# Kernel tuning notes

Hardware: AMD Instinct MI355X
Metric: run time of the kernel (lower is better)

Reference implementation:

```python
import jax, jax.numpy as jnp
import numpy as np

N_BLOCKS = 16
BLOCK = 512  # filters per conv layer
N = N_BLOCKS * BLOCK  # 8192 total nodes (filters)
E = 128  # embedding_feature_len
LAYER_NUM = 2
NEG = -9e15  # matches -9000000000000000.0 zero_vec


def _build_adj():
    filter_num = [BLOCK] * N_BLOCKS
    adj = np.zeros((N, N), dtype=np.float32)
    row = last = filter_num[0]
    for num in filter_num:
        adj[row:row + num, row - last:row] = 1.0
        row += num
        last = num
    np.fill_diagonal(adj, 0.0)
    return adj


def setup_inputs() -> dict:
    key = jax.random.key(0)
    k_h, k_w0, k_w1 = jax.random.split(key, 3)
    h = jax.random.normal(k_h, (N, E), dtype=jnp.float32)
    adj = jnp.asarray(_build_adj())
    s = 1.0 / np.sqrt(E)
    W0 = jax.random.normal(k_w0, (E, E), dtype=jnp.float32) * s
    b0 = jnp.zeros((E,), dtype=jnp.float32)
    W1 = jax.random.normal(k_w1, (E, E), dtype=jnp.float32) * s
    b1 = jnp.zeros((E,), dtype=jnp.float32)
    return {"h": h, "adj": adj, "W0": W0, "b0": b0, "W1": W1, "b1": b1}


def _gat_layer(h, adj, W, b):
    n, e = h.shape
    # attention = h @ h.T / sqrt(E)
    att = jnp.matmul(h, h.T) / jnp.sqrt(jnp.asarray(e, h.dtype))
    A = jnp.where(adj > 0, att, jnp.asarray(NEG, h.dtype))
    A = jax.nn.softmax(A, axis=1)
    # A = (A + I) / 2, without materializing a dense NxN eye
    d = jnp.arange(n)
    A = A * 0.5
    A = A.at[d, d].add(0.5)
    # rows [:num_filter_1layer] overridden with identity rows
    nf1 = jnp.sum(adj[:, 0] != 0)
    mask = d < nf1  # [N]
    A = jnp.where(mask[:, None], 0.0, A)
    A = A.at[d, d].set(jnp.where(mask, 1.0, A[d, d]))
    h_new = jnp.matmul(h, W.T) + b  # nn.Linear
    return jax.nn.relu(jnp.matmul(A, h_new))


def reference(h, adj, W0, b0, W1, b1):
    x = _gat_layer(h, adj, W0, b0)
    x = _gat_layer(x, adj, W1, b1)
    return x
```

## Files before the change

kernel.cpp:

```cpp
#include <hip/hip_runtime.h>

typedef __attribute__((ext_vector_type(4))) float f32x4;
typedef __attribute__((ext_vector_type(8))) short s16x8;
typedef unsigned int u32;
typedef __attribute__((ext_vector_type(2))) u32 u32x2;
typedef __attribute__((ext_vector_type(4))) u32 u32x4;

#define NN 8192
#define EE 128
#define SCLOG2E 0.12751743f

__device__ __forceinline__ ushort f2bf(float f){
  u32 u = __builtin_bit_cast(u32, f);
  u += 0x7fffu + ((u >> 16) & 1u);
  return (ushort)(u >> 16);
}
__device__ __forceinline__ float bf2f(ushort h){
  u32 u = ((u32)h) << 16;
  return __builtin_bit_cast(float, u);
}
__device__ __forceinline__ void gload16(const void* g, void* l){
  __builtin_amdgcn_global_load_lds((const __attribute__((address_space(1))) u32*)g,
                                   (__attribute__((address_space(3))) u32*)l, 16, 0, 0);
}
#define VM_WAIT0   do{ asm volatile("s_waitcnt vmcnt(0)" ::: "memory"); __builtin_amdgcn_sched_barrier(0);}while(0)
#define LGKM_WAIT0 do{ asm volatile("s_waitcnt lgkmcnt(0)" ::: "memory"); __builtin_amdgcn_sched_barrier(0);}while(0)

__global__ __launch_bounds__(256) void prep_k(const float* __restrict__ h,
                                              const float* __restrict__ W0,
                                              const float* __restrict__ W1,
                                              ushort* __restrict__ hhi,
                                              ushort* __restrict__ w0h, ushort* __restrict__ w1h){
  const int b = blockIdx.x, t = threadIdx.x;
  if (b < 128){
    const int base = b*64*EE;
    #pragma unroll
    for (int i=0;i<16;++i){
      int idx = (i*256 + t)*2;
      float2 v = *(const float2*)&h[base + idx];
      *(u32*)&hhi[base + idx] = (u32)f2bf(v.x) | ((u32)f2bf(v.y) << 16);
    }
  } else {
    const float* Ws = (b==128) ? W0 : W1;
    ushort* Wd = (b==128) ? w0h : w1h;
    #pragma unroll
    for (int i=0;i<32;++i){
      int idx = (i*256 + t)*2;
      float2 v = *(const float2*)&Ws[idx];
      *(u32*)&Wd[idx] = (u32)f2bf(v.x) | ((u32)f2bf(v.y) << 16);
    }
  }
}

template<int LAYER>
__global__ __launch_bounds__(256, 1) void gat_k(
    const ushort* __restrict__ Qsrc,
    const ushort* __restrict__ Xsrc,
    const ushort* __restrict__ Wb, const float* __restrict__ bias,
    ushort* __restrict__ Ybf,
    float* __restrict__ Yf)
{
  __shared__ __align__(16) char smem[76288];
  const int t = threadIdx.x;
  const int wv = t >> 6, l = t & 63, lr = l & 15, lg = l >> 4;
  const int wid = ((blockIdx.x & 7) << 5) | (blockIdx.x >> 3);
  const u32 chkoff = wv*8192;
  char* PB = smem + 65536 + wv*2560;
  float* Ls = (float*)(smem + 75776);
  char* AG = smem + 65536;

  const int idx = wid - 16;
  const int rb = (wid < 16) ? wid*32 : 512 + (idx>>4)*512 + (idx&15)*32;
  s16x8 af[2][4];

  if (wid >= 16){
    const int pbase = (idx >> 4) * 512;

    s16x8 qh[2][4];
    #pragma unroll
    for (int h2=0;h2<2;++h2)
      #pragma unroll
      for (int kb=0;kb<4;++kb)
        qh[h2][kb] = *(const s16x8*)&Qsrc[(rb+h2*16+lr)*EE + kb*32 + lg*8];

    const ushort* srcrow = &Xsrc[((l>>3)*4 + ((l&7)>>1))*EE + (l&1)*8];
    auto stage = [&](int c){
      const ushort* src = srcrow + (pbase + c*32)*EE;
      #pragma unroll
      for (int it=0; it<8; ++it)
        gload16(src + it*16, smem + chkoff + it*1024);
    };

    f32x4 O[2][8];
    #pragma unroll
    for (int h2=0;h2<2;++h2)
      #pragma unroll
      for (int nt=0;nt<8;++nt) O[h2][nt] = (f32x4){0.f,0.f,0.f,0.f};
    float lsum[2][4] = {{0.f,0.f,0.f,0.f},{0.f,0.f,0.f,0.f}};

    const u32 trbase = chkoff + (u32)((l>>4)*256 + (l&15)*8);

    stage(wv*4);
    for (int tc=0; tc<4; ++tc){
      VM_WAIT0;

      s16x8 kf[2][4];
      #pragma unroll
      for (int pt=0;pt<2;++pt)
        #pragma unroll
        for (int kb=0;kb<4;++kb)
          kf[pt][kb] = *(const s16x8*)(smem + chkoff + (kb*2+(lg>>1))*1024
                         + (pt*4 + (lr>>2))*128 + (lr&3)*32 + (lg&1)*16);

      s16x8 vf[8];
      #pragma unroll
      for (int nt=0;nt<8;++nt){
        u32x2 a, b;
        u32 off = trbase + (u32)(nt*1024);
        asm volatile("ds_read_b64_tr_b16 %0, %2\n\t"
                     "ds_read_b64_tr_b16 %1, %2 offset:128"
                     : "=&v"(a), "=&v"(b) : "v"(off));
        u32x4 c4; c4[0]=a[0]; c4[1]=a[1]; c4[2]=b[0]; c4[3]=b[1];
        vf[nt] = __builtin_bit_cast(s16x8, c4);
      }
      LGKM_WAIT0;
      if (tc < 3) stage(wv*4 + tc + 1);

      f32x4 sv[2][2];
      __builtin_amdgcn_s_setprio(1);
      #pragma unroll
      for (int h2=0;h2<2;++h2)
        #pragma unroll
        for (int pt=0;pt<2;++pt){
          f32x4 s = (f32x4){0.f,0.f,0.f,0.f};
          #pragma unroll
          for (int kb=0;kb<4;++kb)
            s = __builtin_amdgcn_mfma_f32_16x16x32_bf16(qh[h2][kb], kf[pt][kb], s, 0,0,0);
          sv[h2][pt] = s;
        }
      __builtin_amdgcn_s_setprio(0);

      #pragma unroll
      for (int h2=0;h2<2;++h2)
        #pragma unroll
        for (int r=0;r<4;++r){
          float e0 = exp2f(sv[h2][0][r]*SCLOG2E);
          float e1 = exp2f(sv[h2][1][r]*SCLOG2E);
          sv[h2][0][r] = e0; sv[h2][1][r] = e1;
          lsum[h2][r] += e0 + e1;
        }
      #pragma unroll
      for (int h2=0;h2<2;++h2)
        #pragma unroll
        for (int pt=0;pt<2;++pt)
          #pragma unroll
          for (int r=0;r<4;++r)
            *(ushort*)(PB + h2*1280 + (lg*4+r)*80 + (lr + pt*16)*2) = f2bf(sv[h2][pt][r]);
      s16x8 pf[2];
      #pragma unroll
      for (int h2=0;h2<2;++h2)
        pf[h2] = *(const s16x8*)(PB + h2*1280 + lr*80 + lg*16);
      __builtin_amdgcn_s_setprio(1);
      #pragma unroll
      for (int h2=0;h2<2;++h2)
        #pragma unroll
        for (int nt=0;nt<8;++nt)
          O[h2][nt] = __builtin_amdgcn_mfma_f32_16x16x32_bf16(pf[h2], vf[nt], O[h2][nt], 0,0,0);
      __builtin_amdgcn_s_setprio(0);
    }

    #pragma unroll
    for (int h2=0;h2<2;++h2)
      #pragma unroll
      for (int r=0;r<4;++r){
        float s = lsum[h2][r];
        #pragma unroll
        for (int off=1; off<16; off<<=1) s += __shfl_xor(s, off, 16);
        lsum[h2][r] = s;
      }
    #pragma unroll
    for (int h2=0;h2<2;++h2)
      #pragma unroll
      for (int nt=0;nt<8;++nt)
        *(f32x4*)(smem + h2*32768 + wv*8192 + nt*1024 + l*16) = O[h2][nt];
    if (lr == 0){
      #pragma unroll
      for (int h2=0;h2<2;++h2)
        #pragma unroll
        for (int r=0;r<4;++r) Ls[h2*64 + wv*16 + lg*4 + r] = lsum[h2][r];
    }
    __syncthreads();

    f32x4 om[2][2][4];
    #pragma unroll
    for (int h2=0;h2<2;++h2)
      #pragma unroll
      for (int ntl=0;ntl<2;++ntl){
        int nt = wv*2 + ntl;
        #pragma unroll
        for (int r2=0;r2<4;++r2)
          om[h2][ntl][r2] = *(const f32x4*)(smem + h2*32768 + r2*8192 + nt*1024 + l*16);
      }
    float L[2][4];
    #pragma unroll
    for (int h2=0;h2<2;++h2)
      #pragma unroll
      for (int r=0;r<4;++r){
        int q = lg*4 + r;
        L[h2][r] = Ls[h2*64+q] + Ls[h2*64+16+q] + Ls[h2*64+32+q] + Ls[h2*64+48+q];
      }
    __syncthreads();

    #pragma unroll
    for (int h2=0;h2<2;++h2)
      #pragma unroll
      for (int ntl=0;ntl<2;++ntl){
        int nt = wv*2 + ntl;
        int col = nt*16 + lr;
        #pragma unroll
        for (int r=0;r<4;++r){
          int row = rb + h2*16 + lg*4 + r;
          float qc = bf2f(Qsrc[row*EE + col]);
          float s4 = om[h2][ntl][0][r]+om[h2][ntl][1][r]+om[h2][ntl][2][r]+om[h2][ntl][3][r];
          float agg = 0.5f*qc + 0.5f*(s4 / L[h2][r]);
          int q = h2*16 + lg*4 + r;
          *(ushort*)(AG + q*256 + (((col>>3) ^ (q&7))*16) + (col&7)*2) = f2bf(agg);
        }
      }
    __syncthreads();
    #pragma unroll
    for (int h2=0;h2<2;++h2)
      #pragma unroll
      for (int kb=0;kb<4;++kb)
        af[h2][kb] = *(const s16x8*)(AG + (h2*16+lr)*256 + (((kb*4+lg) ^ (lr&7))*16));
  } else {
    #pragma unroll
    for (int h2=0;h2<2;++h2)
      #pragma unroll
      for (int kb=0;kb<4;++kb)
        af[h2][kb] = *(const s16x8*)&Qsrc[(rb + h2*16 + lr)*EE + kb*32 + lg*8];
  }

  f32x4 acc[2][2];
  #pragma unroll
  for (int h2=0;h2<2;++h2){ acc[h2][0]=(f32x4){0.f,0.f,0.f,0.f}; acc[h2][1]=(f32x4){0.f,0.f,0.f,0.f}; }
  #pragma unroll
  for (int ntl=0;ntl<2;++ntl)
    #pragma unroll
    for (int kb=0;kb<4;++kb){
      s16x8 wb = *(const s16x8*)&Wb[(wv*32 + ntl*16 + lr)*EE + kb*32 + lg*8];
      #pragma unroll
      for (int h2=0;h2<2;++h2)
        acc[h2][ntl] = __builtin_amdgcn_mfma_f32_16x16x32_bf16(af[h2][kb], wb, acc[h2][ntl], 0,0,0);
    }
  #pragma unroll
  for (int h2=0;h2<2;++h2)
    #pragma unroll
    for (int ntl=0;ntl<2;++ntl){
      int col = wv*32 + ntl*16 + lr;
      float bv = bias[col];
      #pragma unroll
      for (int r=0;r<4;++r){
        int row = rb + h2*16 + lg*4 + r;
        float v = fmaxf(acc[h2][ntl][r] + bv, 0.f);
        if constexpr (LAYER == 1) Ybf[row*EE + col] = f2bf(v);
        else                      Yf[row*EE + col] = v;
      }
    }
}

extern "C" void kernel_launch(void* const* d_in, const int* in_sizes, int n_in,
                              void* d_out, int out_size, void* d_ws, size_t ws_size,
                              hipStream_t stream) {
  const float* h  = (const float*)d_in[0];
  const float* W0 = (const float*)d_in[2];
  const float* b0 = (const float*)d_in[3];
  const float* W1 = (const float*)d_in[4];
  const float* b1 = (const float*)d_in[5];
  float* out = (float*)d_out;

  ushort* hhi  = (ushort*)d_ws;
  ushort* w0h  = hhi  + NN*EE;
  ushort* w1h  = w0h  + EE*EE;
  ushort* X1hi = w1h  + EE*EE;

  prep_k<<<130, 256, 0, stream>>>(h, W0, W1, hhi, w0h, w1h);
  gat_k<1><<<256, 256, 0, stream>>>(hhi, hhi, w0h, b0, X1hi, nullptr);
  gat_k<2><<<256, 256, 0, stream>>>(X1hi, X1hi, w1h, b1, nullptr, out);
}
```

Before: 30.42 us.

## Fuse layer-2 identity rows into layer-1 kernel and shrink layer-2 grid

The first 512 rows are identity rows in both layers, so layer 1 now finishes them: it writes its bf16 output into a swizzled LDS tile, runs the second linear (W1, b1) with ReLU, and stores the final fp32 output directly. Layer 2 then launches only 240 blocks, all on the banded attention rows, and its block-to-row mapping is changed to match. The prep kernel is split into twice as many smaller blocks to spread the bf16 conversion over more CUs. This cuts layer-2 launch size and tail work, at the cost of extra work and a barrier in 16 of the layer-1 blocks.

```diff
diff --git a/kernel.cpp b/kernel.cpp
--- a/kernel.cpp
+++ b/kernel.cpp
@@ -32,17 +32,17 @@
                                               ushort* __restrict__ hhi,
                                               ushort* __restrict__ w0h, ushort* __restrict__ w1h){
   const int b = blockIdx.x, t = threadIdx.x;
-  if (b < 128){
-    const int base = b*64*EE;
-    #pragma unroll
-    for (int i=0;i<16;++i){
+  if (b < 256){
+    const int base = b*32*EE;
+    #pragma unroll
+    for (int i=0;i<8;++i){
       int idx = (i*256 + t)*2;
       float2 v = *(const float2*)&h[base + idx];
       *(u32*)&hhi[base + idx] = (u32)f2bf(v.x) | ((u32)f2bf(v.y) << 16);
     }
   } else {
-    const float* Ws = (b==128) ? W0 : W1;
-    ushort* Wd = (b==128) ? w0h : w1h;
+    const float* Ws = (b==256) ? W0 : W1;
+    ushort* Wd = (b==256) ? w0h : w1h;
     #pragma unroll
     for (int i=0;i<32;++i){
       int idx = (i*256 + t)*2;
@@ -57,23 +57,27 @@
     const ushort* __restrict__ Qsrc,
     const ushort* __restrict__ Xsrc,
     const ushort* __restrict__ Wb, const float* __restrict__ bias,
+    const ushort* __restrict__ W2b, const float* __restrict__ bias2,
     ushort* __restrict__ Ybf,
     float* __restrict__ Yf)
 {
   __shared__ __align__(16) char smem[76288];
   const int t = threadIdx.x;
   const int wv = t >> 6, l = t & 63, lr = l & 15, lg = l >> 4;
-  const int wid = ((blockIdx.x & 7) << 5) | (blockIdx.x >> 3);
+  const int bid = blockIdx.x;
+  const int wid = (LAYER == 1) ? (((bid & 7) << 5) | (bid >> 3))
+                               : ((bid & 7)*30 + (bid >> 3));
   const u32 chkoff = wv*8192;
   char* PB = smem + 65536 + wv*2560;
   float* Ls = (float*)(smem + 75776);
   char* AG = smem + 65536;
 
-  const int idx = wid - 16;
-  const int rb = (wid < 16) ? wid*32 : 512 + (idx>>4)*512 + (idx&15)*32;
+  const int idx = (LAYER == 1) ? wid - 16 : wid;
+  const bool banded = (LAYER == 2) || (wid >= 16);
+  const int rb = banded ? 512 + (idx>>4)*512 + (idx&15)*32 : wid*32;
   s16x8 af[2][4];
 
-  if (wid >= 16){
+  if (banded){
     const int pbase = (idx >> 4) * 512;
 
     s16x8 qh[2][4];
@@ -263,10 +267,54 @@
       for (int r=0;r<4;++r){
         int row = rb + h2*16 + lg*4 + r;
         float v = fmaxf(acc[h2][ntl][r] + bv, 0.f);
-        if constexpr (LAYER == 1) Ybf[row*EE + col] = f2bf(v);
-        else                      Yf[row*EE + col] = v;
-      }
-    }
+        if constexpr (LAYER == 1){
+          ushort hi = f2bf(v);
+          Ybf[row*EE + col] = hi;
+          if (!banded){
+            int q = h2*16 + lg*4 + r;
+            *(ushort*)(AG + q*256 + (((col>>3) ^ (q&7))*16) + (col&7)*2) = hi;
+          }
+        } else {
+          Yf[row*EE + col] = v;
+        }
+      }
+    }
+
+  if constexpr (LAYER == 1){
+    if (!banded){
+      __syncthreads();
+      s16x8 af2[2][4];
+      #pragma unroll
+      for (int h2=0;h2<2;++h2)
+        #pragma unroll
+        for (int kb=0;kb<4;++kb)
+          af2[h2][kb] = *(const s16x8*)(AG + (h2*16+lr)*256 + (((kb*4+lg) ^ (lr&7))*16));
+      f32x4 a2[2][2];
+      #pragma unroll
+      for (int h2=0;h2<2;++h2){ a2[h2][0]=(f32x4){0.f,0.f,0.f,0.f}; a2[h2][1]=(f32x4){0.f,0.f,0.f,0.f}; }
+      #pragma unroll
+      for (int ntl=0;ntl<2;++ntl)
+        #pragma unroll
+        for (int kb=0;kb<4;++kb){
+          s16x8 wb = *(const s16x8*)&W2b[(wv*32 + ntl*16 + lr)*EE + kb*32 + lg*8];
+          #pragma unroll
+          for (int h2=0;h2<2;++h2)
+            a2[h2][ntl] = __builtin_amdgcn_mfma_f32_16x16x32_bf16(af2[h2][kb], wb, a2[h2][ntl], 0,0,0);
+        }
+      #pragma unroll
+      for (int h2=0;h2<2;++h2)
+        #pragma unroll
+        for (int ntl=0;ntl<2;++ntl){
+          int col = wv*32 + ntl*16 + lr;
+          float bv = bias2[col];
+          #pragma unroll
+          for (int r=0;r<4;++r){
+            int row = rb + h2*16 + lg*4 + r;
+            Yf[row*EE + col] = fmaxf(a2[h2][ntl][r] + bv, 0.f);
+          }
+        }
+    }
+  }
 }
 
 extern "C" void kernel_launch(void* const* d_in, const int* in_sizes, int n_in,
@@ -284,7 +332,7 @@
   ushort* w1h  = w0h  + EE*EE;
   ushort* X1hi = w1h  + EE*EE;
 
-  prep_k<<<130, 256, 0, stream>>>(h, W0, W1, hhi, w0h, w1h);
-  gat_k<1><<<256, 256, 0, stream>>>(hhi, hhi, w0h, b0, X1hi, nullptr);
-  gat_k<2><<<256, 256, 0, stream>>>(X1hi, X1hi, w1h, b1, nullptr, out);
-}
+  prep_k<<<258, 256, 0, stream>>>(h, W0, W1, hhi, w0h, w1h);
+  gat_k<1><<<256, 256, 0, stream>>>(hhi, hhi, w0h, b0, w1h, b1, X1hi, out);
+  gat_k<2><<<240, 256, 0, stream>>>(X1hi, X1hi, w1h, b1, nullptr, nullptr, nullptr, out);
+}
```

New measurement: 31.36 us. 3.1% more time.

## Fuse fp32-to-bf16 conversion into GAT kernels and drop prep kernel

Applied to the files above, without the earlier changes.

Removes the separate prep kernel that converted h and the weights to bf16. Layer 1 now loads fp32 h directly, converting in registers and writing bf16 into LDS with a register double-buffered staging pipeline instead of async global-to-LDS loads. Both layers convert the fp32 weights on the fly. This saves one kernel launch and a full round trip of h through memory, at the cost of more VGPR pressure, redundant conversion of the same rows across blocks, and a loss of the async LDS loads in layer 1.

```diff
diff --git a/kernel.cpp b/kernel.cpp
--- a/kernel.cpp
+++ b/kernel.cpp
@@ -25,40 +25,15 @@
 }
 #define VM_WAIT0   do{ asm volatile("s_waitcnt vmcnt(0)" ::: "memory"); __builtin_amdgcn_sched_barrier(0);}while(0)
 #define LGKM_WAIT0 do{ asm volatile("s_waitcnt lgkmcnt(0)" ::: "memory"); __builtin_amdgcn_sched_barrier(0);}while(0)
-
-__global__ __launch_bounds__(256) void prep_k(const float* __restrict__ h,
-                                              const float* __restrict__ W0,
-                                              const float* __restrict__ W1,
-                                              ushort* __restrict__ hhi,
-                                              ushort* __restrict__ w0h, ushort* __restrict__ w1h){
-  const int b = blockIdx.x, t = threadIdx.x;
-  if (b < 128){
-    const int base = b*64*EE;
-    #pragma unroll
-    for (int i=0;i<16;++i){
-      int idx = (i*256 + t)*2;
-      float2 v = *(const float2*)&h[base + idx];
-      *(u32*)&hhi[base + idx] = (u32)f2bf(v.x) | ((u32)f2bf(v.y) << 16);
-    }
-  } else {
-    const float* Ws = (b==128) ? W0 : W1;
-    ushort* Wd = (b==128) ? w0h : w1h;
-    #pragma unroll
-    for (int i=0;i<32;++i){
-      int idx = (i*256 + t)*2;
-      float2 v = *(const float2*)&Ws[idx];
-      *(u32*)&Wd[idx] = (u32)f2bf(v.x) | ((u32)f2bf(v.y) << 16);
-    }
-  }
-}
+#define CODE_FENCE do{ asm volatile("" ::: "memory"); __builtin_amdgcn_sched_barrier(0);}while(0)
 
 template<int LAYER>
 __global__ __launch_bounds__(256, 1) void gat_k(
-    const ushort* __restrict__ Qsrc,
-    const ushort* __restrict__ Xsrc,
-    const ushort* __restrict__ Wb, const float* __restrict__ bias,
+    const float*  __restrict__ hf,
+    const ushort* __restrict__ Xbf,
+    const float*  __restrict__ Wf, const float* __restrict__ bias,
     ushort* __restrict__ Ybf,
-    float* __restrict__ Yf)
+    float*  __restrict__ Yf)
 {
   __shared__ __align__(16) char smem[76288];
   const int t = threadIdx.x;
@@ -80,17 +55,53 @@
     #pragma unroll
     for (int h2=0;h2<2;++h2)
       #pragma unroll
-      for (int kb=0;kb<4;++kb)
-        qh[h2][kb] = *(const s16x8*)&Qsrc[(rb+h2*16+lr)*EE + kb*32 + lg*8];
-
-    const ushort* srcrow = &Xsrc[((l>>3)*4 + ((l&7)>>1))*EE + (l&1)*8];
-    auto stage = [&](int c){
-      const ushort* src = srcrow + (pbase + c*32)*EE;
+      for (int kb=0;kb<4;++kb){
+        if constexpr (LAYER == 1){
+          f32x4 a0 = *(const f32x4*)&hf[(rb+h2*16+lr)*EE + kb*32 + lg*8];
+          f32x4 a1 = *(const f32x4*)&hf[(rb+h2*16+lr)*EE + kb*32 + lg*8 + 4];
+          #pragma unroll
+          for (int j=0;j<4;++j){
+            qh[h2][kb][j]   = (short)f2bf(a0[j]);
+            qh[h2][kb][j+4] = (short)f2bf(a1[j]);
+          }
+        } else {
+          qh[h2][kb] = *(const s16x8*)&Xbf[(rb+h2*16+lr)*EE + kb*32 + lg*8];
+        }
+      }
+
+    const int srow = (l>>3)*4 + ((l&7)>>1);
+    const int scol = (l&1)*8;
+
+    const ushort* srcrow2 = (LAYER == 2) ? &Xbf[srow*EE + scol] : nullptr;
+    auto stage2 = [&](int c){
+      const ushort* src = srcrow2 + (pbase + c*32)*EE;
       #pragma unroll
       for (int it=0; it<8; ++it)
         gload16(src + it*16, smem + chkoff + it*1024);
     };
 
+    const float* srcrow1 = (LAYER == 1) ? &hf[srow*EE + scol] : nullptr;
+    f32x4 stg[8][2];
+    auto ldissue = [&](int c){
+      const float* src = srcrow1 + (pbase + c*32)*EE;
+      #pragma unroll
+      for (int it=0; it<8; ++it){
+        stg[it][0] = *(const f32x4*)(src + it*16);
+        stg[it][1] = *(const f32x4*)(src + it*16 + 4);
+      }
+    };
+    auto cvwrite = [&](){
+      #pragma unroll
+      for (int it=0; it<8; ++it){
+        u32x4 pk;
+        pk[0] = (u32)f2bf(stg[it][0][0]) | ((u32)f2bf(stg[it][0][1]) << 16);
+        pk[1] = (u32)f2bf(stg[it][0][2]) | ((u32)f2bf(stg[it][0][3]) << 16);
+        pk[2] = (u32)f2bf(stg[it][1][0]) | ((u32)f2bf(stg[it][1][1]) << 16);
+        pk[3] = (u32)f2bf(stg[it][1][2]) | ((u32)f2bf(stg[it][1][3]) << 16);
+        *(u32x4*)(smem + chkoff + it*1024 + l*16) = pk;
+      }
+    };
+
     f32x4 O[2][8];
     #pragma unroll
     for (int h2=0;h2<2;++h2)
@@ -100,9 +111,17 @@
 
     const u32 trbase = chkoff + (u32)((l>>4)*256 + (l&15)*8);
 
-    stage(wv*4);
+    if constexpr (LAYER == 1){
+      ldissue(wv*4);
+      cvwrite();
+      ldissue(wv*4 + 1);
+      CODE_FENCE;
+    } else {
+      stage2(wv*4);
+    }
+
     for (int tc=0; tc<4; ++tc){
-      VM_WAIT0;
+      if constexpr (LAYER == 2) VM_WAIT0;
 
       s16x8 kf[2][4];
       #pragma unroll
@@ -124,7 +143,16 @@
         vf[nt] = __builtin_bit_cast(s16x8, c4);
       }
       LGKM_WAIT0;
-      if (tc < 3) stage(wv*4 + tc + 1);
+
+      if constexpr (LAYER == 1){
+        if (tc < 3){
+          cvwrite();
+          if (tc < 2) ldissue(wv*4 + tc + 2);
+          CODE_FENCE;
+        }
+      } else {
+        if (tc < 3) stage2(wv*4 + tc + 1);
+      }
 
       f32x4 sv[2][2];
       __builtin_amdgcn_s_setprio(1);
@@ -220,7 +248,9 @@
         #pragma unroll
         for (int r=0;r<4;++r){
           int row = rb + h2*16 + lg*4 + r;
-          float qc = bf2f(Qsrc[row*EE + col]);
+          float qc;
+          if constexpr (LAYER == 1) qc = hf[row*EE + col];
+          else                      qc = bf2f(Xbf[row*EE + col]);
           float s4 = om[h2][ntl][0][r]+om[h2][ntl][1][r]+om[h2][ntl][2][r]+om[h2][ntl][3][r];
           float agg = 0.5f*qc + 0.5f*(s4 / L[h2][r]);
           int q = h2*16 + lg*4 + r;
@@ -237,8 +267,19 @@
     #pragma unroll
     for (int h2=0;h2<2;++h2)
       #pragma unroll
-      for (int kb=0;kb<4;++kb)
-        af[h2][kb] = *(const s16x8*)&Qsrc[(rb + h2*16 + lr)*EE + kb*32 + lg*8];
+      for (int kb=0;kb<4;++kb){
+        if constexpr (LAYER == 1){
+          f32x4 a0 = *(const f32x4*)&hf[(rb+h2*16+lr)*EE + kb*32 + lg*8];
+          f32x4 a1 = *(const f32x4*)&hf[(rb+h2*16+lr)*EE + kb*32 + lg*8 + 4];
+          #pragma unroll
+          for (int j=0;j<4;++j){
+            af[h2][kb][j]   = (short)f2bf(a0[j]);
+            af[h2][kb][j+4] = (short)f2bf(a1[j]);
+          }
+        } else {
+          af[h2][kb] = *(const s16x8*)&Xbf[(rb + h2*16 + lr)*EE + kb*32 + lg*8];
+        }
+      }
   }
 
   f32x4 acc[2][2];
@@ -248,7 +289,11 @@
   for (int ntl=0;ntl<2;++ntl)
     #pragma unroll
     for (int kb=0;kb<4;++kb){
-      s16x8 wb = *(const s16x8*)&Wb[(wv*32 + ntl*16 + lr)*EE + kb*32 + lg*8];
+      f32x4 w0 = *(const f32x4*)&Wf[(wv*32 + ntl*16 + lr)*EE + kb*32 + lg*8];
+      f32x4 w1 = *(const f32x4*)&Wf[(wv*32 + ntl*16 + lr)*EE + kb*32 + lg*8 + 4];
+      s16x8 wb;
+      #pragma unroll
+      for (int j=0;j<4;++j){ wb[j] = (short)f2bf(w0[j]); wb[j+4] = (short)f2bf(w1[j]); }
       #pragma unroll
       for (int h2=0;h2<2;++h2)
         acc[h2][ntl] = __builtin_amdgcn_mfma_f32_16x16x32_bf16(af[h2][kb], wb, acc[h2][ntl], 0,0,0);
@@ -279,12 +324,8 @@
   const float* b1 = (const float*)d_in[5];
   float* out = (float*)d_out;
 
-  ushort* hhi  = (ushort*)d_ws;
-  ushort* w0h  = hhi  + NN*EE;
-  ushort* w1h  = w0h  + EE*EE;
-  ushort* X1hi = w1h  + EE*EE;
-
-  prep_k<<<130, 256, 0, stream>>>(h, W0, W1, hhi, w0h, w1h);
-  gat_k<1><<<256, 256, 0, stream>>>(hhi, hhi, w0h, b0, X1hi, nullptr);
-  gat_k<2><<<256, 256, 0, stream>>>(X1hi, X1hi, w1h, b1, nullptr, out);
-}
+  ushort* X1hi = (ushort*)d_ws;
+
+  gat_k<1><<<256, 256, 0, stream>>>(h, nullptr, W0, b0, X1hi, nullptr);
+  gat_k<2><<<256, 256, 0, stream>>>(nullptr, X1hi, W1, b1, nullptr, out);
+}
```

Result: no change. 30.19 us (-0.8%).
